# Kernel optimization log

Measured on AMD Instinct MI355X. Metric: run time of the kernel, lower is better.

The kernel has to match this reference:

```python
import jax, jax.numpy as jnp
import numpy as np

EPS = 1e-8


def setup_inputs() -> dict:
    key = jax.random.key(0)
    ks = jax.random.split(key, 9)
    b, f, n1, n2 = 32, 256, 64, 256
    inp = {
        "search_feats": jax.random.normal(ks[0], (b, f, n2), jnp.float32),
        "template_feats": jax.random.normal(ks[1], (b, f, n1), jnp.float32),
        "template_seeds": jax.random.normal(ks[2], (b, n1, 3), jnp.float32),
        # SharedMLP (1x1 conv2d) weights: channels 260 -> 256 -> 256 -> 256
        "W1": jax.random.normal(ks[3], (256, 260), jnp.float32) * 0.05,
        "b1": jnp.zeros((256,), jnp.float32),
        "W2": jax.random.normal(ks[4], (256, 256), jnp.float32) * 0.05,
        "b2": jnp.zeros((256,), jnp.float32),
        "W3": jax.random.normal(ks[5], (256, 256), jnp.float32) * 0.05,
        "b3": jnp.zeros((256,), jnp.float32),
        # conv1d chain (kernel size 1): 256 -> 256 (ReLU) -> 256 (no act)
        "W4": jax.random.normal(ks[6], (256, 256), jnp.float32) * 0.05,
        "b4": jnp.zeros((256,), jnp.float32),
        "W5": jax.random.normal(ks[7], (256, 256), jnp.float32) * 0.05,
        "b5": jnp.zeros((256,), jnp.float32),
    }
    return inp


def reference(search_feats, template_feats, template_seeds,
              W1, b1, W2, b2, W3, b3, W4, b4, W5, b5):
    b, f, n2 = search_feats.shape
    n1 = template_feats.shape[-1]

    # Cosine similarity along feature dim (torch clamps each norm to eps).
    t_norm = template_feats / jnp.maximum(
        jnp.linalg.norm(template_feats, axis=1, keepdims=True), EPS)
    s_norm = search_feats / jnp.maximum(
        jnp.linalg.norm(search_feats, axis=1, keepdims=True), EPS)
    sim = jnp.einsum('bfn,bfm->bnm', t_norm, s_norm)  # (b, n1, n2)

    # Build fusion feature (b, 1+3+f, n1, n2) via broadcasting (no copies needed).
    xyz = jnp.transpose(template_seeds, (0, 2, 1))  # (b, 3, n1)
    xyz_b = jnp.broadcast_to(xyz[:, :, :, None], (b, 3, n1, n2))
    tf_b = jnp.broadcast_to(template_feats[:, :, :, None], (b, f, n1, n2))
    fusion = jnp.concatenate([sim[:, None], xyz_b, tf_b], axis=1)  # (b, 260, n1, n2)

    # SharedMLP: 1x1 conv2d + ReLU per layer
    x = jax.nn.relu(jnp.einsum('oc,bcnm->bonm', W1, fusion) + b1[None, :, None, None])
    x = jax.nn.relu(jnp.einsum('oc,bcnm->bonm', W2, x) + b2[None, :, None, None])
    x = jax.nn.relu(jnp.einsum('oc,bcnm->bonm', W3, x) + b3[None, :, None, None])

    # max_pool2d over n1 dim (kernel [n1, 1]) then squeeze -> (b, 256, n2)
    x = jnp.max(x, axis=2)

    # conv1d chain (kernel size 1)
    x = jax.nn.relu(jnp.einsum('oc,bcm->bom', W4, x) + b4[None, :, None])
    x = jnp.einsum('oc,bcm->bom', W5, x) + b5[None, :, None]
    return x
```

## Files before the change

### kernel.cpp

```cpp
#include <hip/hip_runtime.h>
#include <math.h>

#define BB 32
#define FF 256
#define N1 64
#define N2 256

typedef _Float16 f16;
typedef __fp16 h16x2 __attribute__((ext_vector_type(2)));
typedef _Float16 f16x4 __attribute__((ext_vector_type(4)));
typedef _Float16 f16x8 __attribute__((ext_vector_type(8)));
typedef float f32x4 __attribute__((ext_vector_type(4)));

#define OFFB_W14T 0u
#define OFFB_W1H  45056u
#define OFFB_W2H  176128u
#define OFFB_W3H  307200u
#define OFFB_W4H  438272u
#define OFFB_W5H  569344u

__global__ void k_prep(const float* __restrict__ W1, const float* __restrict__ W2,
                       const float* __restrict__ W3, const float* __restrict__ W4,
                       const float* __restrict__ W5, char* __restrict__ wsb) {
  int o = blockIdx.x, k = threadIdx.x;
  int idx = o * 256 + k;
  ((f16*)(wsb + OFFB_W2H))[idx] = (f16)W2[idx];
  ((f16*)(wsb + OFFB_W3H))[idx] = (f16)W3[idx];
  ((f16*)(wsb + OFFB_W4H))[idx] = (f16)W4[idx];
  ((f16*)(wsb + OFFB_W5H))[idx] = (f16)W5[idx];
  ((f16*)(wsb + OFFB_W1H))[idx] = (f16)W1[o * 260 + 4 + k];
  if (k < 4) ((float*)(wsb + OFFB_W14T))[k * 256 + o] = W1[o * 260 + k];
}


#define ZERO_ACC                                                  \
  _Pragma("unroll") for (int of = 0; of < 2; ++of)                \
  _Pragma("unroll") for (int mf = 0; mf < 2; ++mf)                \
      acc[of][mf] = (f32x4){0.f, 0.f, 0.f, 0.f};

#define GEMM2(SRC)                                                                \
  {                                                                               \
    f16x8 bfa0 = *(const f16x8*)((SRC) + 0 * 1024 + lane * 16);                   \
    f16x8 bfa1 = *(const f16x8*)((SRC) + 1 * 1024 + lane * 16);                   \
    __builtin_amdgcn_s_setprio(1);                                                \
    _Pragma("unroll") for (int ks = 0; ks < 8; ++ks) {                            \
      f16x8 bfb0 = bfa0, bfb1 = bfa1;                                             \
      if (ks < 7) {                                                               \
        bfb0 = *(const f16x8*)((SRC) + ((ks + 1) * 2 + 0) * 1024 + lane * 16);    \
        bfb1 = *(const f16x8*)((SRC) + ((ks + 1) * 2 + 1) * 1024 + lane * 16);    \
      }                                                                           \
      _Pragma("unroll") for (int of = 0; of < 2; ++of) {                          \
        acc[of][0] = __builtin_amdgcn_mfma_f32_16x16x32_f16(wreg[of][ks], bfa0,   \
                                                            acc[of][0], 0, 0, 0); \
        acc[of][1] = __builtin_amdgcn_mfma_f32_16x16x32_f16(wreg[of][ks], bfa1,   \
                                                            acc[of][1], 0, 0, 0); \
      }                                                                           \
      bfa0 = bfb0; bfa1 = bfb1;                                                   \
    }                                                                             \
    __builtin_amdgcn_s_setprio(0);                                                \
  }

#define LOAD_WREG(WH)                                                             \
  _Pragma("unroll") for (int of = 0; of < 2; ++of)                                \
  _Pragma("unroll") for (int ks = 0; ks < 8; ++ks)                                \
      wreg[of][ks] = *(const f16x8*)((WH) + (wg * 32 + of * 16 + r) * 256 +       \
                                     ks * 32 + g * 8);

#define STORE_FRAG(DST, BIASP)                                                    \
  _Pragma("unroll") for (int of = 0; of < 2; ++of) {                              \
    f32x4 bv = *(const f32x4*)((BIASP) + wg * 32 + of * 16 + g * 4);              \
    _Pragma("unroll") for (int mf = 0; mf < 2; ++mf) {                            \
      union { h16x2 p[2]; f16x4 v; } u_;                                          \
      u_.p[0] = __builtin_amdgcn_cvt_pkrtz(fmaxf(acc[of][mf][0] + bv[0], 0.f),    \
                                           fmaxf(acc[of][mf][1] + bv[1], 0.f));   \
      u_.p[1] = __builtin_amdgcn_cvt_pkrtz(fmaxf(acc[of][mf][2] + bv[2], 0.f),    \
                                           fmaxf(acc[of][mf][3] + bv[3], 0.f));   \
      *(f16x4*)((DST) + (wg * 2 + mf) * 1024 + (of * 2 + (g >> 1)) * 256 +        \
                r * 16 + (g & 1) * 8) = u_.v;                                     \
    }                                                                             \
  }

#define POOLUP(BIASP)                                                             \
  _Pragma("unroll") for (int of = 0; of < 2; ++of) {                              \
    f32x4 bv = *(const f32x4*)((BIASP) + wg * 32 + of * 16 + g * 4);              \
    _Pragma("unroll") for (int mf = 0; mf < 2; ++mf) {                            \
      union { h16x2 p[2]; f16x4 v; } u_;                                          \
      u_.p[0] = __builtin_amdgcn_cvt_pkrtz(acc[of][mf][0] + bv[0],                \
                                           acc[of][mf][1] + bv[1]);               \
      u_.p[1] = __builtin_amdgcn_cvt_pkrtz(acc[of][mf][2] + bv[2],                \
                                           acc[of][mf][3] + bv[3]);               \
      pool[of][mf] = __builtin_elementwise_max(pool[of][mf], u_.v);               \
    }                                                                             \
  }

#define PRODUCE_Y1(NN, DST)                                                       \
  {                                                                               \
    float simv = sml[(NN) * 32 + mp * 16 + r];                                    \
    f16x8 c8 = *(const f16x8*)(c1h + (NN) * 264 + kp * 32 + g * 8);               \
    float v_[8];                                                                  \
    _Pragma("unroll") for (int q = 0; q < 4; ++q) {                               \
      v_[q] = fmaxf(fmaf(w1a[q], simv, (float)c8[q]), 0.f);                       \
      v_[4 + q] = fmaxf(fmaf(w1b[q], simv, (float)c8[4 + q]), 0.f);               \
    }                                                                             \
    union { h16x2 p[4]; f16x8 v; } u_;                                            \
    u_.p[0] = __builtin_amdgcn_cvt_pkrtz(v_[0], v_[1]);                           \
    u_.p[1] = __builtin_amdgcn_cvt_pkrtz(v_[2], v_[3]);                           \
    u_.p[2] = __builtin_amdgcn_cvt_pkrtz(v_[4], v_[5]);                           \
    u_.p[3] = __builtin_amdgcn_cvt_pkrtz(v_[6], v_[7]);                           \
    *(f16x8*)((DST) + w * 1024 + lane * 16) = u_.v;                               \
  }

__global__ __launch_bounds__(1024, 4) void k_mega(
    const float* __restrict__ sf, const float* __restrict__ tf,
    const float* __restrict__ seeds, const float* __restrict__ b1,
    const float* __restrict__ b2, const float* __restrict__ b3,
    const float* __restrict__ b4, const float* __restrict__ b5,
    const char* __restrict__ wsb, float* __restrict__ out) {
  const int mt = blockIdx.y, b = blockIdx.x, mb = mt * 32;
  const int tid = threadIdx.x;
  const int w = tid >> 6, lane = tid & 63, g = lane >> 4, r = lane & 15;
  const int grp = w >> 3, wg = w & 7;
  const int kp = w >> 1, mp = w & 1;

  const float* w14t = (const float*)(wsb + OFFB_W14T);
  const f16* w1h = (const f16*)(wsb + OFFB_W1H);
  const f16* w2h = (const f16*)(wsb + OFFB_W2H);
  const f16* w3h = (const f16*)(wsb + OFFB_W3H);
  const f16* w4h = (const f16*)(wsb + OFFB_W4H);
  const f16* w5h = (const f16*)(wsb + OFFB_W5H);

  __shared__ __align__(16) char arena[112384];
#define Y1BUF(i) (arena + (i) * 16384)
#define Y2BUF(i) (arena + 32768 + (i) * 16384)
  f16* c1h = (f16*)(arena + 65536);
  float* sml = (float*)(arena + 99328);
  float* blds = (float*)(arena + 107520);
  float* invt_l = (float*)(arena + 111616);
  float* invs_l = (float*)(arena + 111872);
  float* part_t = (float*)(arena + 49152);
  float* part_s = (float*)(arena + 53248);

  {
    const int n = tid & 63, fo = tid >> 6;
    float ssq = 0.f;
#pragma unroll
    for (int j = 0; j < 2; ++j) {
      int oct = j * 16 + fo;
      f16x8 h;
#pragma unroll
      for (int e = 0; e < 8; ++e) {
        float v = tf[((size_t)b * FF + oct * 8 + e) * N1 + n];
        ssq = fmaf(v, v, ssq);
        h[e] = (f16)v;
      }
      *(f16x8*)(arena + ((oct >> 2) * 4 + (n >> 4)) * 1024 +
                ((oct & 3) * 16 + (n & 15)) * 16) = h;
    }
    part_t[n * 16 + fo] = ssq;
  }
  {
    const int m = tid & 31, q = tid >> 5;
    float ssq = 0.f;
    f16x8 h;
#pragma unroll
    for (int e = 0; e < 8; ++e) {
      float v = sf[((size_t)b * FF + q * 8 + e) * N2 + mb + m];
      ssq = fmaf(v, v, ssq);
      h[e] = (f16)v;
    }
    *(f16x8*)(arena + 32768 + ((q >> 2) * 2 + (m >> 4)) * 1024 +
              ((q & 3) * 16 + (m & 15)) * 16) = h;
    part_s[m * 32 + q] = ssq;
  }
  if (tid < 256) {
    blds[tid] = b2[tid];
    blds[256 + tid] = b3[tid];
    blds[512 + tid] = b4[tid];
    blds[768 + tid] = b5[tid];
  }
  __syncthreads();
  if (tid < 64) {
    float a = 0.f;
#pragma unroll
    for (int i = 0; i < 16; ++i) a += part_t[tid * 16 + i];
    invt_l[tid] = 1.0f / fmaxf(sqrtf(a), 1e-8f);
  }
  if (tid < 32) {
    float a = 0.f;
#pragma unroll
    for (int i = 0; i < 32; ++i) a += part_s[tid * 32 + i];
    invs_l[tid] = 1.0f / fmaxf(sqrtf(a), 1e-8f);
  }
  __syncthreads();

  if (w < 8) {
    const int nt = w >> 1, mfs = w & 1;
    f32x4 sa = {0.f, 0.f, 0.f, 0.f};
#pragma unroll
    for (int ks = 0; ks < 8; ++ks) {
      f16x8 af = *(const f16x8*)(arena + (ks * 4 + nt) * 1024 + lane * 16);
      f16x8 bfm = *(const f16x8*)(arena + 32768 + (ks * 2 + mfs) * 1024 + lane * 16);
      sa = __builtin_amdgcn_mfma_f32_16x16x32_f16(af, bfm, sa, 0, 0, 0);
    }
    float ivm = invs_l[mfs * 16 + r];
#pragma unroll
    for (int j = 0; j < 4; ++j) {
      int n = nt * 16 + g * 4 + j;
      sml[n * 32 + mfs * 16 + r] = sa[j] * invt_l[n] * ivm;
    }
  }
  {
    f32x4 ac[4];
#pragma unroll
    for (int nf = 0; nf < 4; ++nf) ac[nf] = (f32x4){0.f, 0.f, 0.f, 0.f};
#pragma unroll 1
    for (int half = 0; half < 2; ++half) {
      f16x8 w1f[4];
#pragma unroll
      for (int kk = 0; kk < 4; ++kk)
        w1f[kk] = *(const f16x8*)(w1h + (w * 16 + r) * 256 +
                                  (half * 4 + kk) * 32 + g * 8);
#pragma unroll
      for (int kk = 0; kk < 4; ++kk)
#pragma unroll
        for (int nf = 0; nf < 4; ++nf) {
          f16x8 bfm = *(const f16x8*)(arena + ((half * 4 + kk) * 4 + nf) * 1024 +
                                      lane * 16);
          ac[nf] =
              __builtin_amdgcn_mfma_f32_16x16x32_f16(w1f[kk], bfm, ac[nf], 0, 0, 0);
        }
    }
    f32x4 b1v = *(const f32x4*)(b1 + w * 16 + g * 4);
    f32x4 wx = *(const f32x4*)(w14t + 256 + w * 16 + g * 4);
    f32x4 wy = *(const f32x4*)(w14t + 512 + w * 16 + g * 4);
    f32x4 wz = *(const f32x4*)(w14t + 768 + w * 16 + g * 4);
#pragma unroll
    for (int nf = 0; nf < 4; ++nf) {
      int n = nf * 16 + r;
      const float* sd = seeds + ((size_t)b * 64 + n) * 3;
      float sx = sd[0], sy = sd[1], sz = sd[2];
      f16x4 hv;
#pragma unroll
      for (int j = 0; j < 4; ++j)
        hv[j] = (f16)(ac[nf][j] + b1v[j] + wx[j] * sx + wy[j] * sy + wz[j] * sz);
      *(f16x4*)(c1h + n * 264 + w * 16 + g * 4) = hv;
    }
  }
  __syncthreads();

  f16x8 wreg[2][8];
  f16x4 pool[2][2];
  f32x4 acc[2][2];
  f32x4 w1a, w1b;
  if (grp) { LOAD_WREG(w3h); } else { LOAD_WREG(w2h); }
  w1a = *(const f32x4*)(w14t + kp * 32 + g * 8);
  w1b = *(const f32x4*)(w14t + kp * 32 + g * 8 + 4);
#pragma unroll
  for (int of = 0; of < 2; ++of)
#pragma unroll
    for (int mf = 0; mf < 2; ++mf) pool[of][mf] = (f16x4){0, 0, 0, 0};

  PRODUCE_Y1(0, Y1BUF(0));
  __syncthreads();

  const float* bA = blds;
  const float* bB = blds + 256;

  for (int n = 0; n < N1; ++n) {
    if (grp == 0) {
      ZERO_ACC;
      GEMM2(Y1BUF(n & 1));
      STORE_FRAG(Y2BUF(n & 1), bA);
      if (n + 1 < N1) PRODUCE_Y1(n + 1, Y1BUF((n + 1) & 1));
    } else {
      if (n + 1 < N1) PRODUCE_Y1(n + 1, Y1BUF((n + 1) & 1));
      if (n > 0) {
        ZERO_ACC;
        GEMM2(Y2BUF((n - 1) & 1));
        POOLUP(bB);
      }
    }
    __syncthreads();
  }

  if (grp == 1) {
    ZERO_ACC;
    GEMM2(Y2BUF(1));
    POOLUP(bB);
#pragma unroll
    for (int of = 0; of < 2; ++of)
#pragma unroll
      for (int mf = 0; mf < 2; ++mf)
        *(f16x4*)(Y1BUF(0) + (wg * 2 + mf) * 1024 + (of * 2 + (g >> 1)) * 256 +
                  r * 16 + (g & 1) * 8) = pool[of][mf];
  } else {
    LOAD_WREG(w4h);
  }
  __syncthreads();
  if (grp == 0) {
    ZERO_ACC;
    GEMM2(Y1BUF(0));
    STORE_FRAG(Y2BUF(0), blds + 512);
  } else {
    LOAD_WREG(w5h);
  }
  __syncthreads();
  if (grp == 1) {
    ZERO_ACC;
    GEMM2(Y2BUF(0));
#pragma unroll
    for (int of = 0; of < 2; ++of) {
      f32x4 bv = *(const f32x4*)(blds + 768 + wg * 32 + of * 16 + g * 4);
#pragma unroll
      for (int mf = 0; mf < 2; ++mf) {
        float* op = out + ((size_t)(b * 256 + wg * 32 + of * 16 + g * 4)) * 256 +
                    mb + mf * 16 + r;
#pragma unroll
        for (int j = 0; j < 4; ++j)
          op[(size_t)j * 256] = acc[of][mf][j] + bv[j];
      }
    }
  }
}

extern "C" void kernel_launch(void* const* d_in, const int* in_sizes, int n_in,
                              void* d_out, int out_size, void* d_ws, size_t ws_size,
                              hipStream_t stream) {
  const float* sf = (const float*)d_in[0];
  const float* tf = (const float*)d_in[1];
  const float* seeds = (const float*)d_in[2];
  const float* W1 = (const float*)d_in[3];
  const float* b1 = (const float*)d_in[4];
  const float* W2 = (const float*)d_in[5];
  const float* b2 = (const float*)d_in[6];
  const float* W3 = (const float*)d_in[7];
  const float* b3 = (const float*)d_in[8];
  const float* W4 = (const float*)d_in[9];
  const float* b4 = (const float*)d_in[10];
  const float* W5 = (const float*)d_in[11];
  const float* b5 = (const float*)d_in[12];
  char* wsb = (char*)d_ws;
  float* out = (float*)d_out;

  k_prep<<<dim3(256), 256, 0, stream>>>(W1, W2, W3, W4, W5, wsb);
  k_mega<<<dim3(BB, 8), 1024, 0, stream>>>(sf, tf, seeds, b1, b2, b3, b4, b5,
                                           wsb, out);
}
```

Measured before the change: 127.0 us.

## Process two n1 rows per barrier with 4-deep LDS ring and global c1 staging

The main n1 loop now handles two rows per iteration, halving the number of block-wide barriers, with the Y1 and Y2 LDS buffers widened from double to quadruple buffering. The per-batch layer-1 constant rows (c1) are written to a global workspace region. One wave streams them into a small 4-row LDS ring ahead of use, freeing LDS for the deeper buffers. This trades fewer synchronisations for more LDS use (about 146 KB per block) and an extra global round-trip. It also relies on global writes being visible within the block after a barrier, and on the workspace being large enough.

Measured after the change: 129.7 us. 1.02x slower.

```diff
diff --git a/kernel.cpp b/kernel.cpp
--- a/kernel.cpp
+++ b/kernel.cpp
@@ -18,6 +18,7 @@
 #define OFFB_W3H  307200u
 #define OFFB_W4H  438272u
 #define OFFB_W5H  569344u
+#define OFFB_C1G  700416u
 
 __global__ void k_prep(const float* __restrict__ W1, const float* __restrict__ W2,
                        const float* __restrict__ W3, const float* __restrict__ W4,
@@ -93,10 +94,10 @@
     }                                                                             \
   }
 
-#define PRODUCE_Y1(NN, DST)                                                       \
+#define PRODUCE_ROW(NN)                                                           \
   {                                                                               \
     float simv = sml[(NN) * 32 + mp * 16 + r];                                    \
-    f16x8 c8 = *(const f16x8*)(c1h + (NN) * 264 + kp * 32 + g * 8);               \
+    f16x8 c8 = *(const f16x8*)(c1r + ((NN) & 3) * 256 + kp * 32 + g * 8);         \
     float v_[8];                                                                  \
     _Pragma("unroll") for (int q = 0; q < 4; ++q) {                               \
       v_[q] = fmaxf(fmaf(w1a[q], simv, (float)c8[q]), 0.f);                       \
@@ -107,7 +108,7 @@
     u_.p[1] = __builtin_amdgcn_cvt_pkrtz(v_[2], v_[3]);                           \
     u_.p[2] = __builtin_amdgcn_cvt_pkrtz(v_[4], v_[5]);                           \
     u_.p[3] = __builtin_amdgcn_cvt_pkrtz(v_[6], v_[7]);                           \
-    *(f16x8*)((DST) + w * 1024 + lane * 16) = u_.v;                               \
+    *(f16x8*)(Y1S(NN) + w * 1024 + lane * 16) = u_.v;                             \
   }
 
 __global__ __launch_bounds__(1024, 4) void k_mega(
@@ -115,7 +116,7 @@
     const float* __restrict__ seeds, const float* __restrict__ b1,
     const float* __restrict__ b2, const float* __restrict__ b3,
     const float* __restrict__ b4, const float* __restrict__ b5,
-    const char* __restrict__ wsb, float* __restrict__ out) {
+    char* __restrict__ wsb, float* __restrict__ out) {
   const int mt = blockIdx.y, b = blockIdx.x, mb = mt * 32;
   const int tid = threadIdx.x;
   const int w = tid >> 6, lane = tid & 63, g = lane >> 4, r = lane & 15;
@@ -128,17 +129,18 @@
   const f16* w3h = (const f16*)(wsb + OFFB_W3H);
   const f16* w4h = (const f16*)(wsb + OFFB_W4H);
   const f16* w5h = (const f16*)(wsb + OFFB_W5H);
-
-  __shared__ __align__(16) char arena[112384];
-#define Y1BUF(i) (arena + (i) * 16384)
-#define Y2BUF(i) (arena + 32768 + (i) * 16384)
-  f16* c1h = (f16*)(arena + 65536);
-  float* sml = (float*)(arena + 99328);
-  float* blds = (float*)(arena + 107520);
-  float* invt_l = (float*)(arena + 111616);
-  float* invs_l = (float*)(arena + 111872);
-  float* part_t = (float*)(arena + 49152);
-  float* part_s = (float*)(arena + 53248);
+  f16* c1b = (f16*)(wsb + OFFB_C1G) + (size_t)b * 16384;
+
+  __shared__ __align__(16) char arena[145792];
+#define Y1S(n) (arena + ((n) & 3) * 16384)
+#define Y2S(n) (arena + 65536 + ((n) & 3) * 16384)
+  f16* c1r = (f16*)(arena + 131072);
+  float* sml = (float*)(arena + 133120);
+  float* blds = (float*)(arena + 141312);
+  float* invt_l = (float*)(arena + 145408);
+  float* invs_l = (float*)(arena + 145664);
+  float* part_t = (float*)(arena + 98304);
+  float* part_s = (float*)(arena + 102400);
 
   {
     const int n = tid & 63, fo = tid >> 6;
@@ -168,7 +170,7 @@
       ssq = fmaf(v, v, ssq);
       h[e] = (f16)v;
     }
-    *(f16x8*)(arena + 32768 + ((q >> 2) * 2 + (m >> 4)) * 1024 +
+    *(f16x8*)(arena + 65536 + ((q >> 2) * 2 + (m >> 4)) * 1024 +
               ((q & 3) * 16 + (m & 15)) * 16) = h;
     part_s[m * 32 + q] = ssq;
   }
@@ -199,7 +201,7 @@
 #pragma unroll
     for (int ks = 0; ks < 8; ++ks) {
       f16x8 af = *(const f16x8*)(arena + (ks * 4 + nt) * 1024 + lane * 16);
-      f16x8 bfm = *(const f16x8*)(arena + 32768 + (ks * 2 + mfs) * 1024 + lane * 16);
+      f16x8 bfm = *(const f16x8*)(arena + 65536 + (ks * 2 + mfs) * 1024 + lane * 16);
       sa = __builtin_amdgcn_mfma_f32_16x16x32_f16(af, bfm, sa, 0, 0, 0);
     }
     float ivm = invs_l[mfs * 16 + r];
@@ -243,10 +245,18 @@
 #pragma unroll
       for (int j = 0; j < 4; ++j)
         hv[j] = (f16)(ac[nf][j] + b1v[j] + wx[j] * sx + wy[j] * sy + wz[j] * sz);
-      *(f16x4*)(c1h + n * 264 + w * 16 + g * 4) = hv;
-    }
-  }
-  __syncthreads();
+      *(f16x4*)(c1b + n * 256 + w * 16 + g * 4) = hv;
+    }
+  }
+  __syncthreads();
+
+  if (w == 15) {
+    int row = lane >> 4;
+    int col = (lane & 15) * 16;
+    *(f16x8*)(c1r + row * 256 + col) = *(const f16x8*)(c1b + row * 256 + col);
+    *(f16x8*)(c1r + row * 256 + col + 8) =
+        *(const f16x8*)(c1b + row * 256 + col + 8);
+  }
 
   f16x8 wreg[2][8];
   f16x4 pool[2][2];
@@ -260,38 +270,56 @@
 #pragma unroll
     for (int mf = 0; mf < 2; ++mf) pool[of][mf] = (f16x4){0, 0, 0, 0};
 
-  PRODUCE_Y1(0, Y1BUF(0));
+  __syncthreads();
+  PRODUCE_ROW(0);
+  PRODUCE_ROW(1);
   __syncthreads();
 
   const float* bA = blds;
   const float* bB = blds + 256;
 
-  for (int n = 0; n < N1; ++n) {
+  for (int p = 0; p < 32; ++p) {
+    const int n0 = 2 * p;
     if (grp == 0) {
       ZERO_ACC;
-      GEMM2(Y1BUF(n & 1));
-      STORE_FRAG(Y2BUF(n & 1), bA);
-      if (n + 1 < N1) PRODUCE_Y1(n + 1, Y1BUF((n + 1) & 1));
+      GEMM2(Y1S(n0));
+      STORE_FRAG(Y2S(n0), bA);
+      ZERO_ACC;
+      GEMM2(Y1S(n0 + 1));
+      STORE_FRAG(Y2S(n0 + 1), bA);
+      if (p < 31) { PRODUCE_ROW(n0 + 2); PRODUCE_ROW(n0 + 3); }
     } else {
-      if (n + 1 < N1) PRODUCE_Y1(n + 1, Y1BUF((n + 1) & 1));
-      if (n > 0) {
+      if (p < 31) { PRODUCE_ROW(n0 + 2); PRODUCE_ROW(n0 + 3); }
+      if (p > 0) {
         ZERO_ACC;
-        GEMM2(Y2BUF((n - 1) & 1));
+        GEMM2(Y2S(n0 - 2));
+        POOLUP(bB);
+        ZERO_ACC;
+        GEMM2(Y2S(n0 - 1));
         POOLUP(bB);
       }
+      if (w == 15 && p < 30) {
+        int row = n0 + 4 + (lane >> 5);
+        int col = (lane & 31) * 8;
+        *(f16x8*)(c1r + (row & 3) * 256 + col) =
+            *(const f16x8*)(c1b + row * 256 + col);
+      }
     }
     __syncthreads();
   }
 
   if (grp == 1) {
     ZERO_ACC;
-    GEMM2(Y2BUF(1));
+    GEMM2(Y2S(62));
     POOLUP(bB);
+    ZERO_ACC;
+    GEMM2(Y2S(63));
+    POOLUP(bB);
 #pragma unroll
     for (int of = 0; of < 2; ++of)
 #pragma unroll
       for (int mf = 0; mf < 2; ++mf)
-        *(f16x4*)(Y1BUF(0) + (wg * 2 + mf) * 1024 + (of * 2 + (g >> 1)) * 256 +
+        *(f16x4*)(Y1S(0) + (wg * 2 + mf) * 1024 + (of * 2 + (g >> 1)) * 256 +
                   r * 16 + (g & 1) * 8) = pool[of][mf];
   } else {
     LOAD_WREG(w4h);
@@ -299,15 +327,15 @@
   __syncthreads();
   if (grp == 0) {
     ZERO_ACC;
-    GEMM2(Y1BUF(0));
-    STORE_FRAG(Y2BUF(0), blds + 512);
+    GEMM2(Y1S(0));
+    STORE_FRAG(Y2S(0), blds + 512);
   } else {
     LOAD_WREG(w5h);
   }
   __syncthreads();
   if (grp == 1) {
     ZERO_ACC;
-    GEMM2(Y2BUF(0));
+    GEMM2(Y2S(0));
 #pragma unroll
     for (int of = 0; of < 2; ++of) {
       f32x4 bv = *(const f32x4*)(blds + 768 + wg * 32 + of * 16 + g * 4);
```
